# Performance work log

Hardware: AMD Instinct MI355X
Metric: run time of the kernel (lower is better)

Reference implementation:

```python
import jax, jax.numpy as jnp
import numpy as np

B = 65536      # total rows = env_batch(8192) * n_slave(8)
DIN = 256      # input_shape
H = 64         # slave_hidden_dim
A = 32         # attention_dim
NACT = 14      # n_actions
NS = 8         # n_slave


def setup_inputs() -> dict:
    key = jax.random.key(0)
    ks = jax.random.split(key, 12)
    s = 0.05
    return {
        "obs": jax.random.normal(ks[0], (B, DIN), jnp.float32),
        "hidden_state": jax.random.normal(ks[1], (B, H), jnp.float32),
        "enc_W": jax.random.normal(ks[2], (DIN, H), jnp.float32) * s,
        "enc_b": jnp.zeros((H,), jnp.float32),
        "gru_Wih": jax.random.normal(ks[3], (3 * H, H), jnp.float32) * s,
        "gru_Whh": jax.random.normal(ks[4], (3 * H, H), jnp.float32) * s,
        "gru_bih": jnp.zeros((3 * H,), jnp.float32),
        "gru_bhh": jnp.zeros((3 * H,), jnp.float32),
        "qW": jax.random.normal(ks[5], (H, A), jnp.float32) * s,
        "kW": jax.random.normal(ks[6], (H, A), jnp.float32) * s,
        "vW": jax.random.normal(ks[7], (H, A), jnp.float32) * s,
        "vb": jnp.zeros((A,), jnp.float32),
        "decW": jax.random.normal(ks[8], (H + A, NACT), jnp.float32) * s,
        "decb": jnp.zeros((NACT,), jnp.float32),
        "n_slave": NS,
    }


def reference(obs, hidden_state, enc_W, enc_b, gru_Wih, gru_Whh, gru_bih, gru_bhh,
              qW, kW, vW, vb, decW, decb, n_slave):
    # encoding + ReLU
    x = jax.nn.relu(obs @ enc_W + enc_b)                      # [B, H]
    # torch GRUCell: r,z,n gate order in weight rows
    gx = x @ gru_Wih.T + gru_bih                              # [B, 3H]
    gh = hidden_state @ gru_Whh.T + gru_bhh                   # [B, 3H]
    xr, xz, xn = jnp.split(gx, 3, axis=-1)
    hr, hz, hn = jnp.split(gh, 3, axis=-1)
    r = jax.nn.sigmoid(xr + hr)
    z = jax.nn.sigmoid(xz + hz)
    n = jnp.tanh(xn + r * hn)
    h_out = (1.0 - z) * n + z * hidden_state                  # [B, H]

    Ad = qW.shape[-1]
    q = (h_out @ qW).reshape(-1, n_slave, Ad)                 # [b, n, A]
    k = (h_out @ kW).reshape(-1, n_slave, Ad)
    v = jax.nn.relu(h_out @ vW + vb).reshape(-1, n_slave, Ad)

    # exclude-self attention == diagonal-masked softmax attention
    scores = jnp.einsum('bia,bja->bij', q, k) / jnp.sqrt(jnp.float32(Ad))
    eye = jnp.eye(n_slave, dtype=bool)
    scores = jnp.where(eye, jnp.float32(-1e9), scores)
    attn = jax.nn.softmax(scores, axis=-1)                    # [b, n, n]
    xatt = jnp.einsum('bij,bja->bia', attn, v).reshape(-1, Ad)  # [B, A]

    out = jnp.concatenate([h_out, xatt], axis=-1) @ decW + decb  # [B, n_actions]
    return (out, h_out)
```

## Files before the change

### kernel.cpp

```cpp
#include <hip/hip_runtime.h>


#define NACT 14
#define BTOT 65536

typedef unsigned int  u32;
typedef unsigned short u16;
using short8 = __attribute__((ext_vector_type(8))) short;
using f32x4  = __attribute__((ext_vector_type(4))) float;

#define ENC0 0
#define WIH0 16384
#define WHH0 28672
#define QKV0 40960
#define DEC0 47104
#define WTOT 48640

__device__ u16   g_wbuf[WTOT];
__device__ float g_bias[256];

__device__ __forceinline__ u32 f2bf_rne(float f){
  u32 x = __float_as_uint(f);
  return (x + 0x7fffu + ((x >> 16) & 1u)) >> 16;
}
__device__ __forceinline__ u32 pk2(float a, float b){
  u32 d;
  asm("v_cvt_pk_bf16_f32 %0, %1, %2" : "=v"(d) : "v"(a), "v"(b));
  return d;
}
__device__ __forceinline__ float blo(u32 u){ return __uint_as_float(u << 16); }
__device__ __forceinline__ float bhi(u32 u){ return __uint_as_float(u & 0xffff0000u); }
__device__ __forceinline__ float sigm(float x){ return 1.0f / (1.0f + __expf(-x)); }
__device__ __forceinline__ float tanhp(float x){ return 1.0f - 2.0f / (__expf(2.0f * x) + 1.0f); }
__device__ __forceinline__ short8 as_s8(uint4 v){ union { uint4 u; short8 s; } x; x.u = v; return x.s; }

#define MFMA16(a,b,c) __builtin_amdgcn_mfma_f32_16x16x32_bf16((a),(b),(c),0,0,0)

__global__ void prep(const float* __restrict__ encW, const float* __restrict__ Wih,
                     const float* __restrict__ Whh,  const float* __restrict__ qW,
                     const float* __restrict__ kW,   const float* __restrict__ vW,
                     const float* __restrict__ decW, const float* __restrict__ bih,
                     const float* __restrict__ bhh)
{
  int j = blockIdx.x * 256 + threadIdx.x;
  if (blockIdx.x == 0) {
    int n = threadIdx.x & 63, g = threadIdx.x >> 6;
    float v;
    if      (g == 0) v = bih[n]       + bhh[n];
    else if (g == 1) v = bih[64 + n]  + bhh[64 + n];
    else if (g == 2) v = bih[128 + n];
    else             v = bhh[128 + n];
    g_bias[threadIdx.x] = v;
  }
  if (j >= WTOT) return;
  int pos  = j & 511;
  int lane = pos >> 3, jj = pos & 7;
  int quad = lane >> 4, l16 = lane & 15;
  float val = 0.f;
  if (j < WIH0) {
    int f = j >> 9, ks = f >> 2, t = f & 3;
    int k = ks * 32 + quad * 8 + jj, n = 16 * t + l16;
    val = encW[k * 64 + n];
  } else if (j < WHH0) {
    int f = (j - WIH0) >> 9;
    int u = f / 6, g = (f >> 1) % 3, ks = f & 1;
    int wrow = 64 * g + 16 * u + l16, k = ks * 32 + quad * 8 + jj;
    val = Wih[wrow * 64 + k];
  } else if (j < QKV0) {
    int f = (j - WHH0) >> 9;
    int u = f / 6, g = (f >> 1) % 3, ks = f & 1;
    int wrow = 64 * g + 16 * u + l16, k = ks * 32 + quad * 8 + jj;
    val = Whh[wrow * 64 + k];
  } else if (j < DEC0) {
    int f = (j - QKV0) >> 9, t = f >> 1, ks = f & 1;
    int n = 16 * t + l16, mtx = n >> 5, nn = n & 31;
    int k = ks * 32 + quad * 8 + jj;
    val = (mtx == 0) ? qW[k * 32 + nn] * 0.17677669529663687f
        : (mtx == 1) ? kW[k * 32 + nn] : vW[k * 32 + nn];
  } else {
    int f = (j - DEC0) >> 9;
    int k = f * 32 + quad * 8 + jj, n = l16;
    if (n < 14) val = decW[k * 14 + n];
  }
  g_wbuf[j] = (u16)f2bf_rne(val);
}

__global__ __launch_bounds__(64, 4)
void commslave_main(const float* __restrict__ obs,  const float* __restrict__ hid,
                    const float* __restrict__ encb, const float* __restrict__ vb,
                    const float* __restrict__ decb, float* __restrict__ out)
{
  __shared__ __align__(16) u16 ldsU[4480];

  const int lane = threadIdx.x & 63;
  const int quad = lane >> 4;
  const int l16  = lane & 15;
  const int gr   = blockIdx.x * 16;
  float* Sf = (float*)(ldsU + 2304);

  float4 hv[4];
  #pragma unroll
  for (int i = 0; i < 4; i++) {
    int c = lane + 64 * i;
    hv[i] = ((const float4*)hid)[(size_t)(gr + (c >> 4)) * 16 + (c & 15)];
  }
  float4 pre[2][2];
  {
    const float* ap = obs + (size_t)(gr + l16) * 256 + quad * 8;
    pre[0][0] = *(const float4*)ap;        pre[0][1] = *(const float4*)(ap + 4);
    pre[1][0] = *(const float4*)(ap + 32); pre[1][1] = *(const float4*)(ap + 36);
  }

  #pragma unroll
  for (int i = 0; i < 4; i++) {
    int c = lane + 64 * i;
    int lr = c >> 4, c4 = c & 15;
    *(uint2*)&ldsU[1152 + lr * 72 + c4 * 4] =
        make_uint2(pk2(hv[i].x, hv[i].y), pk2(hv[i].z, hv[i].w));
  }

  f32x4 ce[4];
  #pragma unroll
  for (int t = 0; t < 4; t++) {
    float bv = encb[16 * t + l16];
    ce[t] = (f32x4){bv, bv, bv, bv};
  }
  #pragma unroll
  for (int ks = 0; ks < 8; ks++) {
    const int s = ks & 1;
    float4 a0 = pre[s][0], a1 = pre[s][1];
    short8 a = as_s8(make_uint4(pk2(a0.x, a0.y), pk2(a0.z, a0.w), pk2(a1.x, a1.y), pk2(a1.z, a1.w)));
    if (ks < 6) {
      const float* ap = obs + (size_t)(gr + l16) * 256 + (ks + 2) * 32 + quad * 8;
      pre[s][0] = *(const float4*)ap;
      pre[s][1] = *(const float4*)(ap + 4);
    }
    #pragma unroll
    for (int t = 0; t < 4; t++) {
      short8 b = as_s8(*(const uint4*)&g_wbuf[ENC0 + (ks * 4 + t) * 512 + lane * 8]);
      ce[t] = MFMA16(a, b, ce[t]);
    }
  }
  #pragma unroll
  for (int t = 0; t < 4; t++)
    #pragma unroll
    for (int r = 0; r < 4; r++) {
      float xv = fmaxf(ce[t][r], 0.f);
      ldsU[(quad * 4 + r) * 72 + 16 * t + l16] = (u16)pk2(xv, xv);
    }

  short8 ax[2], ah[2];
  #pragma unroll
  for (int ks = 0; ks < 2; ks++) {
    ax[ks] = *(const short8*)&ldsU[l16 * 72 + ks * 32 + quad * 8];
    ah[ks] = *(const short8*)&ldsU[1152 + l16 * 72 + ks * 32 + quad * 8];
  }
  #pragma unroll 1
  for (int u = 0; u < 4; u++) {
    f32x4 g6[6];
    #pragma unroll
    for (int t = 0; t < 6; t++) g6[t] = (f32x4){0.f, 0.f, 0.f, 0.f};
    #pragma unroll
    for (int g = 0; g < 3; g++) {
      #pragma unroll
      for (int ks = 0; ks < 2; ks++) {
        int f = (u * 3 + g) * 2 + ks;
        short8 bi = as_s8(*(const uint4*)&g_wbuf[WIH0 + f * 512 + lane * 8]);
        short8 bh = as_s8(*(const uint4*)&g_wbuf[WHH0 + f * 512 + lane * 8]);
        g6[g]     = MFMA16(ax[ks], bi, g6[g]);
        g6[3 + g] = MFMA16(ah[ks], bh, g6[3 + g]);
      }
    }
    int nc = 16 * u + l16;
    float brz = g_bias[nc], bzz = g_bias[64 + nc], bni = g_bias[128 + nc], bnh = g_bias[192 + nc];
    float hp[4];
    #pragma unroll
    for (int r = 0; r < 4; r++)
      hp[r] = blo(ldsU[1152 + (quad * 4 + r) * 72 + nc]);
    #pragma unroll
    for (int r = 0; r < 4; r++) {
      float rg = sigm(g6[0][r] + g6[3][r] + brz);
      float zg = sigm(g6[1][r] + g6[4][r] + bzz);
      float nn = tanhp(g6[2][r] + bni + rg * (g6[5][r] + bnh));
      float ho = (1.f - zg) * nn + zg * hp[r];
      ldsU[1152 + (quad * 4 + r) * 72 + nc] = (u16)pk2(ho, ho);
    }
  }

  short8 hx[2];
  #pragma unroll
  for (int ks = 0; ks < 2; ks++)
    hx[ks] = *(const short8*)&ldsU[1152 + l16 * 72 + ks * 32 + quad * 8];
  f32x4 cq[6];
  #pragma unroll
  for (int t = 0; t < 6; t++) {
    float bv = (t >= 4) ? vb[16 * (t - 4) + l16] : 0.f;
    cq[t] = (f32x4){bv, bv, bv, bv};
  }
  #pragma unroll
  for (int ks = 0; ks < 2; ks++)
    #pragma unroll
    for (int t = 0; t < 6; t++) {
      short8 b = as_s8(*(const uint4*)&g_wbuf[QKV0 + (t * 2 + ks) * 512 + lane * 8]);
      cq[t] = MFMA16(hx[ks], b, cq[t]);
    }
  #pragma unroll
  for (int t = 0; t < 4; t++)
    #pragma unroll
    for (int r = 0; r < 4; r++)
      Sf[(quad * 4 + r) * 68 + 16 * t + l16] = cq[t][r];
  #pragma unroll
  for (int t = 4; t < 6; t++)
    #pragma unroll
    for (int r = 0; r < 4; r++)
      ldsU[(quad * 4 + r) * 72 + 32 + 16 * (t - 4) + l16] =
          (u16)pk2(fmaxf(cq[t][r], 0.f), 0.f);

  {
    const int r_l = lane >> 2, s4 = lane & 3;
    const int gb = r_l & ~7, ri = r_l & 7;
    const float* fq = &Sf[r_l * 68];
    float sc[2];
    #pragma unroll
    for (int jj = 0; jj < 2; jj++) {
      int j = 2 * s4 + jj;
      const float* fk = &Sf[(gb + j) * 68 + 32];
      float d = 0.f;
      #pragma unroll
      for (int a4 = 0; a4 < 32; a4 += 4) {
        float4 q4 = *(const float4*)&fq[a4];
        float4 k4 = *(const float4*)&fk[a4];
        d += q4.x * k4.x + q4.y * k4.y + q4.z * k4.z + q4.w * k4.w;
      }
      sc[jj] = (j == ri) ? -1e30f : d;
    }
    float m = fmaxf(sc[0], sc[1]);
    m = fmaxf(m, __shfl_xor(m, 1));
    m = fmaxf(m, __shfl_xor(m, 2));
    float p[2], sum = 0.f;
    #pragma unroll
    for (int jj = 0; jj < 2; jj++) {
      int j = 2 * s4 + jj;
      p[jj] = (j == ri) ? 0.f : __expf(sc[jj] - m);
      sum += p[jj];
    }
    sum += __shfl_xor(sum, 1);
    sum += __shfl_xor(sum, 2);
    float inv = 1.f / sum;
    #pragma unroll
    for (int jj = 0; jj < 2; jj++)
      Sf[r_l * 68 + 2 * s4 + jj] = p[jj] * inv;
    float xa[8];
    #pragma unroll
    for (int u = 0; u < 8; u++) xa[u] = 0.f;
    #pragma unroll
    for (int j = 0; j < 8; j++) {
      float aj = Sf[r_l * 68 + j];
      const u16* vp = &ldsU[(gb + j) * 72 + 32 + 8 * s4];
      uint4 v0 = *(const uint4*)vp;
      xa[0] += aj * blo(v0.x); xa[1] += aj * bhi(v0.x);
      xa[2] += aj * blo(v0.y); xa[3] += aj * bhi(v0.y);
      xa[4] += aj * blo(v0.z); xa[5] += aj * bhi(v0.z);
      xa[6] += aj * blo(v0.w); xa[7] += aj * bhi(v0.w);
    }
    u16* xp = &ldsU[r_l * 72 + 8 * s4];
    *(uint4*)xp = make_uint4(pk2(xa[0], xa[1]), pk2(xa[2], xa[3]),
                             pk2(xa[4], xa[5]), pk2(xa[6], xa[7]));
  }

  {
    float db = (l16 < NACT) ? decb[l16] : 0.f;
    f32x4 co = (f32x4){db, db, db, db};
    #pragma unroll
    for (int ks = 0; ks < 2; ks++) {
      short8 b = as_s8(*(const uint4*)&g_wbuf[DEC0 + ks * 512 + lane * 8]);
      short8 a = *(const short8*)&ldsU[1152 + l16 * 72 + ks * 32 + quad * 8];
      co = MFMA16(a, b, co);
    }
    short8 b2 = as_s8(*(const uint4*)&g_wbuf[DEC0 + 2 * 512 + lane * 8]);
    short8 a2 = *(const short8*)&ldsU[l16 * 72 + quad * 8];
    co = MFMA16(a2, b2, co);
    if (l16 < NACT)
      #pragma unroll
      for (int r = 0; r < 4; r++)
        out[(size_t)(gr + quad * 4 + r) * NACT + l16] = co[r];
  }

  {
    float* outH = out + (size_t)BTOT * NACT;
    #pragma unroll
    for (int i = 0; i < 2; i++) {
      int c = lane + 64 * i, lr = c >> 3, j = c & 7;
      uint4 u = *(const uint4*)&ldsU[1152 + lr * 72 + 8 * j];
      *(float4*)(outH + (size_t)(gr + lr) * 64 + 8 * j) =
          make_float4(blo(u.x), bhi(u.x), blo(u.y), bhi(u.y));
      *(float4*)(outH + (size_t)(gr + lr) * 64 + 8 * j + 4) =
          make_float4(blo(u.z), bhi(u.z), blo(u.w), bhi(u.w));
    }
  }
}

extern "C" void kernel_launch(void* const* d_in, const int* in_sizes, int n_in,
                              void* d_out, int out_size, void* d_ws, size_t ws_size,
                              hipStream_t stream) {
  (void)in_sizes; (void)n_in; (void)d_ws; (void)ws_size; (void)out_size;
  const float* obs  = (const float*)d_in[0];
  const float* hid  = (const float*)d_in[1];
  const float* encW = (const float*)d_in[2];
  const float* encb = (const float*)d_in[3];
  const float* Wih  = (const float*)d_in[4];
  const float* Whh  = (const float*)d_in[5];
  const float* bih  = (const float*)d_in[6];
  const float* bhh  = (const float*)d_in[7];
  const float* qW   = (const float*)d_in[8];
  const float* kW   = (const float*)d_in[9];
  const float* vW   = (const float*)d_in[10];
  const float* vb   = (const float*)d_in[11];
  const float* decW = (const float*)d_in[12];
  const float* decb = (const float*)d_in[13];
  float* out = (float*)d_out;

  prep<<<(WTOT + 255) / 256, 256, 0, stream>>>(encW, Wih, Whh, qW, kW, vW, decW, bih, bhh);
  commslave_main<<<BTOT / 16, 64, 0, stream>>>(obs, hid, encb, vb, decb, out);
}
```

Baseline: 150.3 us.

## Stage GRU/QKV/decoder weights in LDS and process two tiles per wave

New measurement: 147.5 us. About the same (-1.9%).

```diff
diff --git a/kernel.cpp b/kernel.cpp
--- a/kernel.cpp
+++ b/kernel.cpp
@@ -16,8 +16,16 @@
 #define DEC0 47104
 #define WTOT 48640
 
-__device__ u16   g_wbuf[WTOT];
-__device__ float g_bias[256];
+#define WIHL 0
+#define WHHL 12288
+#define QKVL 24576
+#define DECL 30720
+#define DATA0 32256
+#define BIASL 69120
+#define LDSU16 69632
+
+__device__ __align__(16) u16   g_wbuf[WTOT];
+__device__ __align__(16) float g_bias[256];
 
 __device__ __forceinline__ u32 f2bf_rne(float f){
   u32 x = __float_as_uint(f);
@@ -85,18 +93,18 @@
   g_wbuf[j] = (u16)f2bf_rne(val);
 }
 
-__global__ __launch_bounds__(64, 4)
-void commslave_main(const float* __restrict__ obs,  const float* __restrict__ hid,
-                    const float* __restrict__ encb, const float* __restrict__ vb,
-                    const float* __restrict__ decb, float* __restrict__ out)
+template<bool LAST>
+__device__ __forceinline__ void tile_body(
+    int gr, int grN,
+    u16* __restrict__ Xb, const u16* __restrict__ wl, const float* __restrict__ biasL,
+    const float* __restrict__ obs, const float* __restrict__ hid,
+    const float* __restrict__ encb, const float* __restrict__ vb,
+    const float* __restrict__ decb, float* __restrict__ out,
+    float4 (&pre)[2][2], float4 (&preN)[2][2],
+    int lane, int quad, int l16)
 {
-  __shared__ __align__(16) u16 ldsU[4480];
-
-  const int lane = threadIdx.x & 63;
-  const int quad = lane >> 4;
-  const int l16  = lane & 15;
-  const int gr   = blockIdx.x * 16;
-  float* Sf = (float*)(ldsU + 2304);
+  u16*   Hb = Xb + 1152;
+  float* Sf = (float*)(Xb + 2304);
 
   float4 hv[4];
   #pragma unroll
@@ -104,19 +112,11 @@
     int c = lane + 64 * i;
     hv[i] = ((const float4*)hid)[(size_t)(gr + (c >> 4)) * 16 + (c & 15)];
   }
-  float4 pre[2][2];
-  {
-    const float* ap = obs + (size_t)(gr + l16) * 256 + quad * 8;
-    pre[0][0] = *(const float4*)ap;        pre[0][1] = *(const float4*)(ap + 4);
-    pre[1][0] = *(const float4*)(ap + 32); pre[1][1] = *(const float4*)(ap + 36);
-  }
-
   #pragma unroll
   for (int i = 0; i < 4; i++) {
     int c = lane + 64 * i;
     int lr = c >> 4, c4 = c & 15;
-    *(uint2*)&ldsU[1152 + lr * 72 + c4 * 4] =
-        make_uint2(pk2(hv[i].x, hv[i].y), pk2(hv[i].z, hv[i].w));
+    *(uint2*)&Hb[lr * 72 + c4 * 4] = make_uint2(pk2(hv[i].x, hv[i].y), pk2(hv[i].z, hv[i].w));
   }
 
   f32x4 ce[4];
@@ -141,21 +141,26 @@
       ce[t] = MFMA16(a, b, ce[t]);
     }
   }
+  if (!LAST) {
+    const float* ap = obs + (size_t)(grN + l16) * 256 + quad * 8;
+    preN[0][0] = *(const float4*)ap;        preN[0][1] = *(const float4*)(ap + 4);
+    preN[1][0] = *(const float4*)(ap + 32); preN[1][1] = *(const float4*)(ap + 36);
+  }
   #pragma unroll
   for (int t = 0; t < 4; t++)
     #pragma unroll
     for (int r = 0; r < 4; r++) {
       float xv = fmaxf(ce[t][r], 0.f);
-      ldsU[(quad * 4 + r) * 72 + 16 * t + l16] = (u16)pk2(xv, xv);
+      Xb[(quad * 4 + r) * 72 + 16 * t + l16] = (u16)pk2(xv, xv);
     }
 
   short8 ax[2], ah[2];
   #pragma unroll
   for (int ks = 0; ks < 2; ks++) {
-    ax[ks] = *(const short8*)&ldsU[l16 * 72 + ks * 32 + quad * 8];
-    ah[ks] = *(const short8*)&ldsU[1152 + l16 * 72 + ks * 32 + quad * 8];
-  }
-  #pragma unroll 1
+    ax[ks] = *(const short8*)&Xb[l16 * 72 + ks * 32 + quad * 8];
+    ah[ks] = *(const short8*)&Hb[l16 * 72 + ks * 32 + quad * 8];
+  }
+  #pragma unroll
   for (int u = 0; u < 4; u++) {
     f32x4 g6[6];
     #pragma unroll
@@ -165,32 +170,32 @@
       #pragma unroll
       for (int ks = 0; ks < 2; ks++) {
         int f = (u * 3 + g) * 2 + ks;
-        short8 bi = as_s8(*(const uint4*)&g_wbuf[WIH0 + f * 512 + lane * 8]);
-        short8 bh = as_s8(*(const uint4*)&g_wbuf[WHH0 + f * 512 + lane * 8]);
+        short8 bi = *(const short8*)&wl[WIHL + f * 512 + lane * 8];
+        short8 bh = *(const short8*)&wl[WHHL + f * 512 + lane * 8];
         g6[g]     = MFMA16(ax[ks], bi, g6[g]);
         g6[3 + g] = MFMA16(ah[ks], bh, g6[3 + g]);
       }
     }
     int nc = 16 * u + l16;
-    float brz = g_bias[nc], bzz = g_bias[64 + nc], bni = g_bias[128 + nc], bnh = g_bias[192 + nc];
+    float brz = biasL[nc], bzz = biasL[64 + nc], bni = biasL[128 + nc], bnh = biasL[192 + nc];
     float hp[4];
     #pragma unroll
     for (int r = 0; r < 4; r++)
-      hp[r] = blo(ldsU[1152 + (quad * 4 + r) * 72 + nc]);
+      hp[r] = blo(Hb[(quad * 4 + r) * 72 + nc]);
     #pragma unroll
     for (int r = 0; r < 4; r++) {
       float rg = sigm(g6[0][r] + g6[3][r] + brz);
       float zg = sigm(g6[1][r] + g6[4][r] + bzz);
       float nn = tanhp(g6[2][r] + bni + rg * (g6[5][r] + bnh));
       float ho = (1.f - zg) * nn + zg * hp[r];
-      ldsU[1152 + (quad * 4 + r) * 72 + nc] = (u16)pk2(ho, ho);
+      Hb[(quad * 4 + r) * 72 + nc] = (u16)pk2(ho, ho);
     }
   }
 
   short8 hx[2];
   #pragma unroll
   for (int ks = 0; ks < 2; ks++)
-    hx[ks] = *(const short8*)&ldsU[1152 + l16 * 72 + ks * 32 + quad * 8];
+    hx[ks] = *(const short8*)&Hb[l16 * 72 + ks * 32 + quad * 8];
   f32x4 cq[6];
   #pragma unroll
   for (int t = 0; t < 6; t++) {
@@ -201,7 +206,7 @@
   for (int ks = 0; ks < 2; ks++)
     #pragma unroll
     for (int t = 0; t < 6; t++) {
-      short8 b = as_s8(*(const uint4*)&g_wbuf[QKV0 + (t * 2 + ks) * 512 + lane * 8]);
+      short8 b = *(const short8*)&wl[QKVL + (t * 2 + ks) * 512 + lane * 8];
       cq[t] = MFMA16(hx[ks], b, cq[t]);
     }
   #pragma unroll
@@ -213,7 +218,7 @@
   for (int t = 4; t < 6; t++)
     #pragma unroll
     for (int r = 0; r < 4; r++)
-      ldsU[(quad * 4 + r) * 72 + 32 + 16 * (t - 4) + l16] =
+      Xb[(quad * 4 + r) * 72 + 32 + 16 * (t - 4) + l16] =
           (u16)pk2(fmaxf(cq[t][r], 0.f), 0.f);
 
   {
@@ -256,14 +261,14 @@
     #pragma unroll
     for (int j = 0; j < 8; j++) {
       float aj = Sf[r_l * 68 + j];
-      const u16* vp = &ldsU[(gb + j) * 72 + 32 + 8 * s4];
+      const u16* vp = &Xb[(gb + j) * 72 + 32 + 8 * s4];
       uint4 v0 = *(const uint4*)vp;
       xa[0] += aj * blo(v0.x); xa[1] += aj * bhi(v0.x);
       xa[2] += aj * blo(v0.y); xa[3] += aj * bhi(v0.y);
       xa[4] += aj * blo(v0.z); xa[5] += aj * bhi(v0.z);
       xa[6] += aj * blo(v0.w); xa[7] += aj * bhi(v0.w);
     }
-    u16* xp = &ldsU[r_l * 72 + 8 * s4];
+    u16* xp = &Xb[r_l * 72 + 8 * s4];
     *(uint4*)xp = make_uint4(pk2(xa[0], xa[1]), pk2(xa[2], xa[3]),
                              pk2(xa[4], xa[5]), pk2(xa[6], xa[7]));
   }
@@ -273,12 +278,12 @@
     f32x4 co = (f32x4){db, db, db, db};
     #pragma unroll
     for (int ks = 0; ks < 2; ks++) {
-      short8 b = as_s8(*(const uint4*)&g_wbuf[DEC0 + ks * 512 + lane * 8]);
-      short8 a = *(const short8*)&ldsU[1152 + l16 * 72 + ks * 32 + quad * 8];
+      short8 b = *(const short8*)&wl[DECL + ks * 512 + lane * 8];
+      short8 a = *(const short8*)&Hb[l16 * 72 + ks * 32 + quad * 8];
       co = MFMA16(a, b, co);
     }
-    short8 b2 = as_s8(*(const uint4*)&g_wbuf[DEC0 + 2 * 512 + lane * 8]);
-    short8 a2 = *(const short8*)&ldsU[l16 * 72 + quad * 8];
+    short8 b2 = *(const short8*)&wl[DECL + 2 * 512 + lane * 8];
+    short8 a2 = *(const short8*)&Xb[l16 * 72 + quad * 8];
     co = MFMA16(a2, b2, co);
     if (l16 < NACT)
       #pragma unroll
@@ -291,13 +296,57 @@
     #pragma unroll
     for (int i = 0; i < 2; i++) {
       int c = lane + 64 * i, lr = c >> 3, j = c & 7;
-      uint4 u = *(const uint4*)&ldsU[1152 + lr * 72 + 8 * j];
+      uint4 u = *(const uint4*)&Hb[lr * 72 + 8 * j];
       *(float4*)(outH + (size_t)(gr + lr) * 64 + 8 * j) =
           make_float4(blo(u.x), bhi(u.x), blo(u.y), bhi(u.y));
       *(float4*)(outH + (size_t)(gr + lr) * 64 + 8 * j + 4) =
           make_float4(blo(u.z), bhi(u.z), blo(u.w), bhi(u.w));
     }
   }
+}
+
+__global__ __launch_bounds__(512, 2)
+void commslave_main(const float* __restrict__ obs,  const float* __restrict__ hid,
+                    const float* __restrict__ encb, const float* __restrict__ vb,
+                    const float* __restrict__ decb, float* __restrict__ out)
+{
+  __shared__ __align__(16) u16 lds[LDSU16];
+
+  const int tid  = threadIdx.x;
+  const int w    = tid >> 6;
+  const int lane = tid & 63;
+  const int quad = lane >> 4;
+  const int l16  = lane & 15;
+
+  {
+    uint4* dw = (uint4*)lds;
+    const uint4* sw = (const uint4*)(g_wbuf + WIH0);
+    #pragma unroll
+    for (int i = 0; i < 8; i++) {
+      int idx = tid + 512 * i;
+      if (idx < 4032) dw[idx] = sw[idx];
+    }
+    if (tid < 64) ((uint4*)(lds + BIASL))[tid] = ((const uint4*)g_bias)[tid];
+  }
+
+  const int gr0 = blockIdx.x * 256 + w * 16;
+  const int gr1 = gr0 + 128;
+
+  float4 pre0[2][2], pre1[2][2];
+  {
+    const float* ap = obs + (size_t)(gr0 + l16) * 256 + quad * 8;
+    pre0[0][0] = *(const float4*)ap;        pre0[0][1] = *(const float4*)(ap + 4);
+    pre0[1][0] = *(const float4*)(ap + 32); pre0[1][1] = *(const float4*)(ap + 36);
+  }
+  __syncthreads();
+
+  u16* Xb = lds + DATA0 + w * 4608;
+  const float* biasL = (const float*)(lds + BIASL);
+
+  tile_body<false>(gr0, gr1, Xb, lds, biasL, obs, hid, encb, vb, decb, out,
+                   pre0, pre1, lane, quad, l16);
+  tile_body<true >(gr1, 0,   Xb, lds, biasL, obs, hid, encb, vb, decb, out,
+                   pre1, pre0, lane, quad, l16);
 }
 
 extern "C" void kernel_launch(void* const* d_in, const int* in_sizes, int n_in,
@@ -321,5 +370,5 @@
   float* out = (float*)d_out;
 
   prep<<<(WTOT + 255) / 256, 256, 0, stream>>>(encW, Wih, Whh, qW, kW, vW, decW, bih, bhh);
-  commslave_main<<<BTOT / 16, 64, 0, stream>>>(obs, hid, encb, vb, decb, out);
-}
+  commslave_main<<<256, 512, 0, stream>>>(obs, hid, encb, vb, decb, out);
+}
```
